# Optimization experiments

Hardware: AMD Instinct MI355X
Metric: run time of the kernel (lower is better)

## Reference

```python
import jax, jax.numpy as jnp
import numpy as np

B, S, D_IN, D_OUT, CAP = 4, 2048, 4096, 4096, 1024


def setup_inputs() -> dict:
    key = jax.random.key(0)
    k1, k2, k3, k4, k5 = jax.random.split(key, 5)
    x = jax.random.normal(k1, (B, S, D_IN), dtype=jnp.float32)
    # lattice-quantized weights (static buffer) and per-row scale
    weight_lattices = jax.random.normal(k2, (D_OUT, D_IN), dtype=jnp.float32)
    weight_scales = jax.random.uniform(k3, (D_OUT, 1), dtype=jnp.float32)
    # associative LatticeMemory: keys over input dim, values over output dim
    mem_keys = jax.random.normal(k4, (CAP, D_IN), dtype=jnp.float32)
    mem_values = jax.random.normal(k5, (CAP, D_OUT), dtype=jnp.float32)
    return {"x": x, "weight_lattices": weight_lattices,
            "weight_scales": weight_scales,
            "mem_keys": mem_keys, "mem_values": mem_values}


def reference(x, weight_lattices, weight_scales, mem_keys, mem_values):
    # dequantize: elementwise scale of the lattice codes -> full fp32 weight
    w_dequant = weight_lattices * weight_scales            # [O, I]
    # main GEMM: out = x @ w_dequant.T
    out = jnp.einsum('bsi,oi->bso', x, w_dequant)          # [B, S, O]
    # associative memory retrieval on the first flattened token
    q = x.reshape(-1, x.shape[-1])[0]                      # [I]
    attn = jax.nn.softmax(mem_keys @ q)                    # [CAP]
    memory_out = attn @ mem_values                         # [O]
    return out + 0.01 * memory_out
```

## Files before the change

### kernel.cpp

```cpp
#include <hip/hip_runtime.h>
#include <hip/hip_bf16.h>
#include <stdint.h>

#define D_IN   4096
#define D_OUT  4096
#define MROWS  8192
#define CAPN   1024

typedef __bf16 bf16x8 __attribute__((ext_vector_type(8)));
typedef float f32x4 __attribute__((ext_vector_type(4)));

__device__ static inline void async_copy16(const void* g, void* l) {
  __builtin_amdgcn_global_load_lds((__attribute__((address_space(1))) void*)g,
                                   (__attribute__((address_space(3))) void*)l,
                                   16, 0, 0);
}

__global__ __launch_bounds__(256) void cvt_x_kernel(const float* __restrict__ x,
                                                    __hip_bfloat16* __restrict__ xb) {
  size_t i = ((size_t)blockIdx.x * 256 + threadIdx.x) * 8;
  float4 f0 = *(const float4*)(x + i);
  float4 f1 = *(const float4*)(x + i + 4);
  union { __hip_bfloat16 h[8]; uint4 u; } o;
  o.h[0] = __float2bfloat16(f0.x); o.h[1] = __float2bfloat16(f0.y);
  o.h[2] = __float2bfloat16(f0.z); o.h[3] = __float2bfloat16(f0.w);
  o.h[4] = __float2bfloat16(f1.x); o.h[5] = __float2bfloat16(f1.y);
  o.h[6] = __float2bfloat16(f1.z); o.h[7] = __float2bfloat16(f1.w);
  *(uint4*)(xb + i) = o.u;
}

__global__ __launch_bounds__(256) void cvt_w_kernel(const float* __restrict__ wl,
                                                    const float* __restrict__ wscale,
                                                    __hip_bfloat16* __restrict__ wb) {
  size_t i = ((size_t)blockIdx.x * 256 + threadIdx.x) * 8;
  int row = (int)(i >> 12);
  float s = wscale[row];
  float4 f0 = *(const float4*)(wl + i);
  float4 f1 = *(const float4*)(wl + i + 4);
  union { __hip_bfloat16 h[8]; uint4 u; } o;
  o.h[0] = __float2bfloat16(f0.x * s); o.h[1] = __float2bfloat16(f0.y * s);
  o.h[2] = __float2bfloat16(f0.z * s); o.h[3] = __float2bfloat16(f0.w * s);
  o.h[4] = __float2bfloat16(f1.x * s); o.h[5] = __float2bfloat16(f1.y * s);
  o.h[6] = __float2bfloat16(f1.z * s); o.h[7] = __float2bfloat16(f1.w * s);
  *(uint4*)(wb + i) = o.u;
}

__global__ __launch_bounds__(256) void mem_logits_kernel(const float* __restrict__ keys,
                                                         const float* __restrict__ q,
                                                         float* __restrict__ logits) {
  int c = blockIdx.x;
  const float* k = keys + (size_t)c * D_IN;
  float p = 0.f;
  for (int i = threadIdx.x; i < D_IN; i += 256) p += k[i] * q[i];
  for (int off = 32; off; off >>= 1) p += __shfl_down(p, off);
  __shared__ float r[4];
  if ((threadIdx.x & 63) == 0) r[threadIdx.x >> 6] = p;
  __syncthreads();
  if (threadIdx.x == 0) logits[c] = r[0] + r[1] + r[2] + r[3];
}

__global__ __launch_bounds__(1024) void softmax_kernel(const float* __restrict__ logits,
                                                       float* __restrict__ attn) {
  int t = threadIdx.x;
  float v = logits[t];
  float m = v;
  for (int off = 32; off; off >>= 1) m = fmaxf(m, __shfl_down(m, off));
  __shared__ float wm[16];
  __shared__ float smax, ssum;
  if ((t & 63) == 0) wm[t >> 6] = m;
  __syncthreads();
  if (t == 0) {
    float mm = wm[0];
    for (int i = 1; i < 16; i++) mm = fmaxf(mm, wm[i]);
    smax = mm;
  }
  __syncthreads();
  float e = __expf(v - smax);
  float s = e;
  for (int off = 32; off; off >>= 1) s += __shfl_down(s, off);
  __shared__ float wsum[16];
  if ((t & 63) == 0) wsum[t >> 6] = s;
  __syncthreads();
  if (t == 0) {
    float ss = 0.f;
    for (int i = 0; i < 16; i++) ss += wsum[i];
    ssum = ss;
  }
  __syncthreads();
  attn[t] = e / ssum;
}

__global__ __launch_bounds__(256) void mem_out_kernel(const float* __restrict__ attn,
                                                      const float* __restrict__ vals,
                                                      float* __restrict__ memo) {
  int o = blockIdx.x * 256 + threadIdx.x;
  int c0 = blockIdx.y * 64;
  float acc = 0.f;
#pragma unroll 8
  for (int c = c0; c < c0 + 64; c++) acc += attn[c] * vals[(size_t)c * D_OUT + o];
  atomicAdd(&memo[o], acc);
}

__global__ __launch_bounds__(256) void gemm_bt_kernel(const __hip_bfloat16* __restrict__ A,
                                                      const __hip_bfloat16* __restrict__ Bm,
                                                      const float* __restrict__ memo,
                                                      float* __restrict__ C) {
  __shared__ bf16x8 As[2][512];
  __shared__ bf16x8 Bs[2][512];
  const int tid = threadIdx.x;
  const int l = tid & 63;
  const int w = tid >> 6;
  const int m_blk = blockIdx.y * 128;
  const int n_blk = blockIdx.x * 128;

  const int lm = l & 15;
  const int lk = (l >> 4) * 8;

  const __hip_bfloat16* gA0 = A  + (size_t)(m_blk + w * 16 + lm) * D_IN + lk;
  const __hip_bfloat16* gA1 = gA0 + (size_t)64 * D_IN;
  const __hip_bfloat16* gB0 = Bm + (size_t)(n_blk + w * 16 + lm) * D_IN + lk;
  const __hip_bfloat16* gB1 = gB0 + (size_t)64 * D_IN;

  const int wm = (w >> 1) * 4;
  const int wn = (w & 1) * 4;

  async_copy16(gA0, &As[0][w * 64]);
  async_copy16(gA1, &As[0][(w + 4) * 64]);
  async_copy16(gB0, &Bs[0][w * 64]);
  async_copy16(gB1, &Bs[0][(w + 4) * 64]);

  f32x4 acc[4][4] = {};

  for (int k0 = 0; k0 < D_IN / 32; ++k0) {
    const int c = k0 & 1;
    __syncthreads();

    bf16x8 a[4], b[4];
#pragma unroll
    for (int i = 0; i < 4; i++) a[i] = As[c][(wm + i) * 64 + l];
#pragma unroll
    for (int j = 0; j < 4; j++) b[j] = Bs[c][(wn + j) * 64 + l];

    if (k0 + 1 < D_IN / 32) {
      const int nb = c ^ 1;
      const int koff = (k0 + 1) * 32;
      async_copy16(gA0 + koff, &As[nb][w * 64]);
      async_copy16(gA1 + koff, &As[nb][(w + 4) * 64]);
      async_copy16(gB0 + koff, &Bs[nb][w * 64]);
      async_copy16(gB1 + koff, &Bs[nb][(w + 4) * 64]);
    }

#pragma unroll
    for (int i = 0; i < 4; i++)
#pragma unroll
      for (int j = 0; j < 4; j++)
        acc[i][j] = __builtin_amdgcn_mfma_f32_16x16x32_bf16(a[i], b[j], acc[i][j], 0, 0, 0);
  }

  const int col_l = l & 15;
  const int row_l = (l >> 4) * 4;
#pragma unroll
  for (int j = 0; j < 4; j++) {
    int col = n_blk + (wn + j) * 16 + col_l;
    float mo = 0.01f * memo[col];
#pragma unroll
    for (int i = 0; i < 4; i++) {
      int row = m_blk + (wm + i) * 16 + row_l;
      float* cp = C + (size_t)row * D_OUT + col;
#pragma unroll
      for (int r = 0; r < 4; r++) cp[(size_t)r * D_OUT] = acc[i][j][r] + mo;
    }
  }
}

extern "C" void kernel_launch(void* const* d_in, const int* in_sizes, int n_in,
                              void* d_out, int out_size, void* d_ws, size_t ws_size,
                              hipStream_t stream) {
  const float* x   = (const float*)d_in[0];
  const float* wl  = (const float*)d_in[1];
  const float* wsc = (const float*)d_in[2];
  const float* mk  = (const float*)d_in[3];
  const float* mv  = (const float*)d_in[4];
  float* out = (float*)d_out;

  char* wsb = (char*)d_ws;
  __hip_bfloat16* xb = (__hip_bfloat16*)wsb;
  __hip_bfloat16* wb = (__hip_bfloat16*)(wsb + (size_t)MROWS * D_IN * 2);
  float* logits = (float*)(wsb + (size_t)MROWS * D_IN * 2 + (size_t)D_OUT * D_IN * 2);
  float* attn = logits + CAPN;
  float* memo = attn + CAPN;

  cvt_x_kernel<<<dim3((MROWS * D_IN) / 2048), dim3(256), 0, stream>>>(x, xb);
  cvt_w_kernel<<<dim3((D_OUT * D_IN) / 2048), dim3(256), 0, stream>>>(wl, wsc, wb);

  mem_logits_kernel<<<dim3(CAPN), dim3(256), 0, stream>>>(mk, x, logits);
  softmax_kernel<<<dim3(1), dim3(1024), 0, stream>>>(logits, attn);
  hipMemsetAsync(memo, 0, D_OUT * sizeof(float), stream);
  mem_out_kernel<<<dim3(D_OUT / 256, 16), dim3(256), 0, stream>>>(attn, mv, memo);

  gemm_bt_kernel<<<dim3(D_OUT / 128, MROWS / 128), dim3(256), 0, stream>>>(xb, wb, memo, out);
}
```

Measured before the change: 785.4 us.

## Replace GEMM with 256x256 eight-phase pipelined kernel and fuse softmax into memory readout

```diff
diff --git a/kernel.cpp b/kernel.cpp
--- a/kernel.cpp
+++ b/kernel.cpp
@@ -6,6 +6,7 @@
 #define D_OUT  4096
 #define MROWS  8192
 #define CAPN   1024
+#define NT     64
 
 typedef __bf16 bf16x8 __attribute__((ext_vector_type(8)));
 typedef float f32x4 __attribute__((ext_vector_type(4)));
@@ -59,116 +60,156 @@
   if (threadIdx.x == 0) logits[c] = r[0] + r[1] + r[2] + r[3];
 }
 
-__global__ __launch_bounds__(1024) void softmax_kernel(const float* __restrict__ logits,
-                                                       float* __restrict__ attn) {
-  int t = threadIdx.x;
-  float v = logits[t];
-  float m = v;
+__global__ __launch_bounds__(256) void mem_attn_out_kernel(const float* __restrict__ logits,
+                                                           const float* __restrict__ vals,
+                                                           float* __restrict__ memo) {
+  int tid = threadIdx.x;
+  __shared__ float sa[1024];
+  __shared__ float wm[4], ws[4];
+  __shared__ float part[4][64];
+  float4 lv = ((const float4*)logits)[tid];
+  float m = fmaxf(fmaxf(lv.x, lv.y), fmaxf(lv.z, lv.w));
   for (int off = 32; off; off >>= 1) m = fmaxf(m, __shfl_down(m, off));
-  __shared__ float wm[16];
-  __shared__ float smax, ssum;
-  if ((t & 63) == 0) wm[t >> 6] = m;
-  __syncthreads();
-  if (t == 0) {
-    float mm = wm[0];
-    for (int i = 1; i < 16; i++) mm = fmaxf(mm, wm[i]);
-    smax = mm;
-  }
-  __syncthreads();
-  float e = __expf(v - smax);
-  float s = e;
+  if ((tid & 63) == 0) wm[tid >> 6] = m;
+  __syncthreads();
+  m = fmaxf(fmaxf(wm[0], wm[1]), fmaxf(wm[2], wm[3]));
+  float e0 = __expf(lv.x - m), e1 = __expf(lv.y - m);
+  float e2 = __expf(lv.z - m), e3 = __expf(lv.w - m);
+  float s = e0 + e1 + e2 + e3;
   for (int off = 32; off; off >>= 1) s += __shfl_down(s, off);
-  __shared__ float wsum[16];
-  if ((t & 63) == 0) wsum[t >> 6] = s;
-  __syncthreads();
-  if (t == 0) {
-    float ss = 0.f;
-    for (int i = 0; i < 16; i++) ss += wsum[i];
-    ssum = ss;
-  }
-  __syncthreads();
-  attn[t] = e / ssum;
-}
-
-__global__ __launch_bounds__(256) void mem_out_kernel(const float* __restrict__ attn,
-                                                      const float* __restrict__ vals,
-                                                      float* __restrict__ memo) {
-  int o = blockIdx.x * 256 + threadIdx.x;
-  int c0 = blockIdx.y * 64;
+  if ((tid & 63) == 0) ws[tid >> 6] = s;
+  __syncthreads();
+  float inv = 1.f / (ws[0] + ws[1] + ws[2] + ws[3]);
+  sa[tid * 4 + 0] = e0 * inv; sa[tid * 4 + 1] = e1 * inv;
+  sa[tid * 4 + 2] = e2 * inv; sa[tid * 4 + 3] = e3 * inv;
+  __syncthreads();
+  int g = tid >> 6, lane = tid & 63;
+  int o = blockIdx.x * 64 + lane;
   float acc = 0.f;
+  const float* vp = vals + (size_t)(g * 256) * D_OUT + o;
 #pragma unroll 8
-  for (int c = c0; c < c0 + 64; c++) acc += attn[c] * vals[(size_t)c * D_OUT + o];
-  atomicAdd(&memo[o], acc);
-}
-
-__global__ __launch_bounds__(256) void gemm_bt_kernel(const __hip_bfloat16* __restrict__ A,
-                                                      const __hip_bfloat16* __restrict__ Bm,
-                                                      const float* __restrict__ memo,
-                                                      float* __restrict__ C) {
-  __shared__ bf16x8 As[2][512];
-  __shared__ bf16x8 Bs[2][512];
+  for (int c = 0; c < 256; ++c) acc += sa[g * 256 + c] * vp[(size_t)c * D_OUT];
+  part[g][lane] = acc;
+  __syncthreads();
+  if (tid < 64) memo[o] = part[0][lane] + part[1][lane] + part[2][lane] + part[3][lane];
+}
+
+__global__ __launch_bounds__(512, 2) void gemm_8ph_kernel(const __hip_bfloat16* __restrict__ A,
+                                                          const __hip_bfloat16* __restrict__ Bm,
+                                                          const float* __restrict__ memo,
+                                                          float* __restrict__ C) {
+  __shared__ bf16x8 LA[2][32][64];
+  __shared__ bf16x8 LB[2][32][64];
   const int tid = threadIdx.x;
   const int l = tid & 63;
   const int w = tid >> 6;
-  const int m_blk = blockIdx.y * 128;
-  const int n_blk = blockIdx.x * 128;
+  const int wr = w >> 2;
+  const int wc = w & 3;
+  const int w2 = w * 2;
+
+  const int bid = blockIdx.x;
+  const int swz = (bid & 7) * 64 + (bid >> 3);
+  const int m_blk = (swz >> 4) * 256;
+  const int n_blk = (swz & 15) * 256;
 
   const int lm = l & 15;
   const int lk = (l >> 4) * 8;
 
-  const __hip_bfloat16* gA0 = A  + (size_t)(m_blk + w * 16 + lm) * D_IN + lk;
-  const __hip_bfloat16* gA1 = gA0 + (size_t)64 * D_IN;
-  const __hip_bfloat16* gB0 = Bm + (size_t)(n_blk + w * 16 + lm) * D_IN + lk;
-  const __hip_bfloat16* gB1 = gB0 + (size_t)64 * D_IN;
-
-  const int wm = (w >> 1) * 4;
-  const int wn = (w & 1) * 4;
-
-  async_copy16(gA0, &As[0][w * 64]);
-  async_copy16(gA1, &As[0][(w + 4) * 64]);
-  async_copy16(gB0, &Bs[0][w * 64]);
-  async_copy16(gB1, &Bs[0][(w + 4) * 64]);
-
-  f32x4 acc[4][4] = {};
-
-  for (int k0 = 0; k0 < D_IN / 32; ++k0) {
-    const int c = k0 & 1;
-    __syncthreads();
-
-    bf16x8 a[4], b[4];
-#pragma unroll
-    for (int i = 0; i < 4; i++) a[i] = As[c][(wm + i) * 64 + l];
-#pragma unroll
-    for (int j = 0; j < 4; j++) b[j] = Bs[c][(wn + j) * 64 + l];
-
-    if (k0 + 1 < D_IN / 32) {
-      const int nb = c ^ 1;
-      const int koff = (k0 + 1) * 32;
-      async_copy16(gA0 + koff, &As[nb][w * 64]);
-      async_copy16(gA1 + koff, &As[nb][(w + 4) * 64]);
-      async_copy16(gB0 + koff, &Bs[nb][w * 64]);
-      async_copy16(gB1 + koff, &Bs[nb][(w + 4) * 64]);
-    }
-
-#pragma unroll
-    for (int i = 0; i < 4; i++)
-#pragma unroll
-      for (int j = 0; j < 4; j++)
-        acc[i][j] = __builtin_amdgcn_mfma_f32_16x16x32_bf16(a[i], b[j], acc[i][j], 0, 0, 0);
+  const __hip_bfloat16* baseA0 = A  + (size_t)(m_blk + (0 * 8 + w) * 16 + lm) * D_IN + lk;
+  const __hip_bfloat16* baseA1 = A  + (size_t)(m_blk + (1 * 8 + w) * 16 + lm) * D_IN + lk;
+  const __hip_bfloat16* baseB0 = Bm + (size_t)(n_blk + (0 * 8 + w) * 16 + lm) * D_IN + lk;
+  const __hip_bfloat16* baseB1 = Bm + (size_t)(n_blk + (1 * 8 + w) * 16 + lm) * D_IN + lk;
+
+#define STAGE_A(h, T, sb) do {                                                   \
+    async_copy16(baseA##h + (size_t)(T) * 64,      &LA[sb][(h) * 16 + w2][0]);   \
+    async_copy16(baseA##h + (size_t)(T) * 64 + 32, &LA[sb][(h) * 16 + w2 + 1][0]); \
+  } while (0)
+#define STAGE_B(h, T, sb) do {                                                   \
+    async_copy16(baseB##h + (size_t)(T) * 64,      &LB[sb][(h) * 16 + w2][0]);   \
+    async_copy16(baseB##h + (size_t)(T) * 64 + 32, &LB[sb][(h) * 16 + w2 + 1][0]); \
+  } while (0)
+
+  f32x4 acc[8][4] = {};
+  bf16x8 a[4][2], b[4][2];
+
+#define BAR_MFMA(JH, IH)                                                         \
+  do {                                                                           \
+    __builtin_amdgcn_s_barrier();                                                \
+    asm volatile("s_waitcnt lgkmcnt(0)" ::: "memory");                           \
+    __builtin_amdgcn_sched_barrier(0);                                           \
+    __builtin_amdgcn_s_setprio(1);                                               \
+    _Pragma("unroll") for (int jj = 0; jj < 4; ++jj)                             \
+    _Pragma("unroll") for (int i2 = 0; i2 < 2; ++i2)                             \
+    _Pragma("unroll") for (int kk = 0; kk < 2; ++kk)                             \
+      acc[(JH) * 4 + jj][(IH) * 2 + i2] = __builtin_amdgcn_mfma_f32_16x16x32_bf16( \
+          a[jj][kk], b[(IH) * 2 + i2][kk], acc[(JH) * 4 + jj][(IH) * 2 + i2], 0, 0, 0); \
+    __builtin_amdgcn_s_setprio(0);                                               \
+    __builtin_amdgcn_sched_barrier(0);                                           \
+    __builtin_amdgcn_s_barrier();                                                \
+  } while (0)
+
+#define TILE4(t, bb, DOS1, DOS2, VMSTMT)                                         \
+  do {                                                                           \
+                                                                        \
+    _Pragma("unroll") for (int j = 0; j < 4; ++j) {                              \
+      a[j][0] = LA[bb][(2 * j + wr) * 2 + 0][l];                                 \
+      a[j][1] = LA[bb][(2 * j + wr) * 2 + 1][l];                                 \
+    }                                                                            \
+    _Pragma("unroll") for (int ii = 0; ii < 2; ++ii) {                           \
+      b[ii][0] = LB[bb][(4 * ii + wc) * 2 + 0][l];                               \
+      b[ii][1] = LB[bb][(4 * ii + wc) * 2 + 1][l];                               \
+    }                                                                            \
+    if (DOS1) { STAGE_A(1, (t) + 1, (bb) ^ 1); }                                 \
+    BAR_MFMA(0, 0);                                                              \
+                                                                        \
+    _Pragma("unroll") for (int ii = 2; ii < 4; ++ii) {                           \
+      b[ii][0] = LB[bb][(4 * ii + wc) * 2 + 0][l];                               \
+      b[ii][1] = LB[bb][(4 * ii + wc) * 2 + 1][l];                               \
+    }                                                                            \
+    if (DOS2) { STAGE_A(0, (t) + 2, bb); }                                       \
+    BAR_MFMA(0, 1);                                                              \
+                                                                        \
+    _Pragma("unroll") for (int j = 0; j < 4; ++j) {                              \
+      a[j][0] = LA[bb][(2 * j + 8 + wr) * 2 + 0][l];                             \
+      a[j][1] = LA[bb][(2 * j + 8 + wr) * 2 + 1][l];                             \
+    }                                                                            \
+    if (DOS2) { STAGE_B(0, (t) + 2, bb); }                                       \
+    BAR_MFMA(1, 0);                                                              \
+                                                                        \
+    if (DOS2) { STAGE_B(1, (t) + 2, bb); }                                       \
+    VMSTMT;                                                                      \
+    BAR_MFMA(1, 1);                                                              \
+  } while (0)
+
+#define VM6 asm volatile("s_waitcnt vmcnt(6)" ::: "memory")
+#define VM0 asm volatile("s_waitcnt vmcnt(0)" ::: "memory")
+#define VMN ((void)0)
+
+  STAGE_A(0, 0, 0); STAGE_B(0, 0, 0); STAGE_B(1, 0, 0); STAGE_A(1, 0, 0);
+  STAGE_A(0, 1, 1); STAGE_B(0, 1, 1); STAGE_B(1, 1, 1);
+  asm volatile("s_waitcnt vmcnt(6)" ::: "memory");
+  __builtin_amdgcn_s_barrier();
+
+#pragma unroll 1
+  for (int t = 0; t < NT - 2; t += 2) {
+    TILE4(t, 0, 1, 1, VM6);
+    TILE4(t + 1, 1, 1, 1, VM6);
   }
+  TILE4(NT - 2, 0, 1, 0, VM0);
+  TILE4(NT - 1, 1, 0, 0, VMN);
 
   const int col_l = l & 15;
   const int row_l = (l >> 4) * 4;
 #pragma unroll
-  for (int j = 0; j < 4; j++) {
-    int col = n_blk + (wn + j) * 16 + col_l;
+  for (int ii = 0; ii < 4; ++ii) {
+    int col = n_blk + (4 * ii + wc) * 16 + col_l;
     float mo = 0.01f * memo[col];
 #pragma unroll
-    for (int i = 0; i < 4; i++) {
-      int row = m_blk + (wm + i) * 16 + row_l;
+    for (int j = 0; j < 8; ++j) {
+      int row = m_blk + (2 * j + wr) * 16 + row_l;
       float* cp = C + (size_t)row * D_OUT + col;
 #pragma unroll
-      for (int r = 0; r < 4; r++) cp[(size_t)r * D_OUT] = acc[i][j][r] + mo;
+      for (int r = 0; r < 4; ++r) cp[(size_t)r * D_OUT] = acc[j][ii][r] + mo;
     }
   }
 }
@@ -187,16 +228,13 @@
   __hip_bfloat16* xb = (__hip_bfloat16*)wsb;
   __hip_bfloat16* wb = (__hip_bfloat16*)(wsb + (size_t)MROWS * D_IN * 2);
   float* logits = (float*)(wsb + (size_t)MROWS * D_IN * 2 + (size_t)D_OUT * D_IN * 2);
-  float* attn = logits + CAPN;
-  float* memo = attn + CAPN;
+  float* memo = logits + CAPN;
 
   cvt_x_kernel<<<dim3((MROWS * D_IN) / 2048), dim3(256), 0, stream>>>(x, xb);
   cvt_w_kernel<<<dim3((D_OUT * D_IN) / 2048), dim3(256), 0, stream>>>(wl, wsc, wb);
 
   mem_logits_kernel<<<dim3(CAPN), dim3(256), 0, stream>>>(mk, x, logits);
-  softmax_kernel<<<dim3(1), dim3(1024), 0, stream>>>(logits, attn);
-  hipMemsetAsync(memo, 0, D_OUT * sizeof(float), stream);
-  mem_out_kernel<<<dim3(D_OUT / 256, 16), dim3(256), 0, stream>>>(attn, mv, memo);
-
-  gemm_bt_kernel<<<dim3(D_OUT / 128, MROWS / 128), dim3(256), 0, stream>>>(xb, wb, memo, out);
-}
+  mem_attn_out_kernel<<<dim3(D_OUT / 64), dim3(256), 0, stream>>>(logits, mv, memo);
+
+  gemm_8ph_kernel<<<dim3((MROWS / 256) * (D_OUT / 256)), dim3(512), 0, stream>>>(xb, wb, memo, out);
+}
```

Measured after the change: 659.1 us. 16.1% less time.
